# Kernel tuning notes

Hardware: AMD Instinct MI355X
Metric: run time of the kernel (lower is better)

## Reference

```python
import jax, jax.numpy as jnp
import numpy as np

WS = 7          # window size
NWIN = 3        # 2*neig_win_num+1
NH_LOC = 4      # local (POLA) heads
NH_AX = 2       # axial heads per axis
DIM = 256
LC = 128        # local channels = NH_LOC * (DIM//8)
AC = 64         # axial channels per axis
HID = 1024
B = 4
HIMG = 112
WIMG = 112
TBL = ((NWIN + 1) * WS - 1) ** 2  # 729


def _rel_pos_index():
    c = np.stack(np.meshgrid(np.arange(WS), np.arange(WS), indexing='ij')).reshape(2, -1)
    n = np.stack(np.meshgrid(np.arange(NWIN * WS), np.arange(NWIN * WS), indexing='ij')).reshape(2, -1)
    rel = (c[:, :, None] - n[:, None, :]).transpose(1, 2, 0)
    rel[..., 0] += NWIN * WS - 1
    rel[..., 1] += NWIN * WS - 1
    rel[..., 0] *= (NWIN + 1) * WS - 1
    return rel.sum(-1)  # (WS*WS, (NWIN*WS)**2)

REL_IDX = jnp.asarray(_rel_pos_index())


def _ln(x, w, b, eps=1e-5):
    mu = x.mean(-1, keepdims=True)
    var = ((x - mu) ** 2).mean(-1, keepdims=True)
    return (x - mu) * jax.lax.rsqrt(var + eps) * w + b


def _mha(q, k, v, wq, bq, wk, bk, wv, bv, wp, bp, nh, bias=None):
    Bn, Nq, C = q.shape
    d = C // nh
    qh = (q @ wq + bq).reshape(Bn, Nq, nh, d).transpose(0, 2, 1, 3) * (d ** -0.5)
    kh = (k @ wk + bk).reshape(Bn, -1, nh, d).transpose(0, 2, 1, 3)
    vh = (v @ wv + bv).reshape(Bn, -1, nh, d).transpose(0, 2, 1, 3)
    attn = jnp.einsum('bhqd,bhkd->bhqk', qh, kh)
    if bias is not None:
        attn = attn + bias[None]
    attn = jax.nn.softmax(attn, axis=-1)
    out = jnp.einsum('bhqk,bhkd->bhqd', attn, vh)
    out = out.transpose(0, 2, 1, 3).reshape(Bn, Nq, C)
    return out @ wp + bp


def _forward(x, ln1_w, ln1_b, ln2_w, ln2_b, loc_bias_table,
             loc_wq, loc_bq, loc_wk, loc_bk, loc_wv, loc_bv, loc_wp, loc_bp,
             v_wq, v_bq, v_wk, v_bk, v_wv, v_bv, v_wp, v_bp,
             h_wq, h_bq, h_wk, h_bk, h_wv, h_bv, h_wp, h_bp,
             fc1_w, fc1_b, fc2_w, fc2_b, H, W):
    Bx, L, C = x.shape
    shortcut = x
    h1 = _ln(x, ln1_w, ln1_b).reshape(Bx, H, W, C)
    xl, xv, xh = h1[..., :LC], h1[..., LC:LC + AC], h1[..., LC + AC:]
    nH, nW = H // WS, W // WS
    # --- POLA: windowed queries, 3x3-neighbor-window keys/values ---
    qw = xl.reshape(Bx, nH, WS, nW, WS, LC).transpose(0, 1, 3, 2, 4, 5).reshape(Bx * nH * nW, WS * WS, LC)
    xp = jnp.pad(xl, ((0, 0), (WS, WS), (WS, WS), (0, 0)))
    ih = (jnp.arange(nH) * WS)[:, None] + jnp.arange(NWIN * WS)[None, :]   # (nH, 3*WS)
    iw = (jnp.arange(nW) * WS)[:, None] + jnp.arange(NWIN * WS)[None, :]
    kv = xp[:, ih][:, :, :, iw]                                            # (B,nH,3ws,nW,3ws,LC)
    kv = kv.transpose(0, 1, 3, 2, 4, 5).reshape(Bx * nH * nW, (NWIN * WS) ** 2, LC)
    bias = loc_bias_table[REL_IDX].transpose(2, 0, 1)                      # (NH_LOC, 49, 441)
    ol = _mha(qw, kv, kv, loc_wq, loc_bq, loc_wk, loc_bk, loc_wv, loc_bv, loc_wp, loc_bp, NH_LOC, bias)
    ol = ol.reshape(Bx, nH, nW, WS, WS, LC).transpose(0, 1, 3, 2, 4, 5).reshape(Bx, H, W, LC)
    # --- vertical axial attention (along H, per column) ---
    xv2 = xv.transpose(0, 2, 1, 3).reshape(Bx * W, H, AC)
    ov = _mha(xv2, xv2, xv2, v_wq, v_bq, v_wk, v_bk, v_wv, v_bv, v_wp, v_bp, NH_AX)
    ov = ov.reshape(Bx, W, H, AC).transpose(0, 2, 1, 3)
    # --- horizontal axial attention (along W, per row) ---
    xh2 = xh.reshape(Bx * H, W, AC)
    oh = _mha(xh2, xh2, xh2, h_wq, h_bq, h_wk, h_bk, h_wv, h_bv, h_wp, h_bp, NH_AX)
    oh = oh.reshape(Bx, H, W, AC)
    x2 = shortcut + jnp.concatenate([ol, ov, oh], -1).reshape(Bx, L, C)
    h2 = _ln(x2, ln2_w, ln2_b)
    h2 = jax.nn.gelu(h2 @ fc1_w + fc1_b, approximate=False)
    return x2 + (h2 @ fc2_w + fc2_b)


def setup_inputs():
    key = jax.random.key(0)
    ki = iter(jax.random.split(key, 40))
    def w(shape, s=0.02):
        return jax.random.normal(next(ki), shape, jnp.float32) * s
    inp = {
        'x': jax.random.normal(next(ki), (B, HIMG * WIMG, DIM), jnp.float32),
        'H': HIMG, 'W': WIMG,
        'ln1_w': jnp.ones((DIM,), jnp.float32), 'ln1_b': jnp.zeros((DIM,), jnp.float32),
        'ln2_w': jnp.ones((DIM,), jnp.float32), 'ln2_b': jnp.zeros((DIM,), jnp.float32),
        'loc_bias_table': w((TBL, NH_LOC)),
    }
    for p, d in (('loc', LC), ('v', AC), ('h', AC)):
        for n in ('q', 'k', 'v', 'p'):
            inp[p + '_w' + n] = w((d, d))
            inp[p + '_b' + n] = w((d,))
    inp['fc1_w'] = w((DIM, HID)); inp['fc1_b'] = w((HID,))
    inp['fc2_w'] = w((HID, DIM)); inp['fc2_b'] = w((DIM,))
    return inp


def reference(x, ln1_w, ln1_b, ln2_w, ln2_b, loc_bias_table,
              loc_wq, loc_bq, loc_wk, loc_bk, loc_wv, loc_bv, loc_wp, loc_bp,
              v_wq, v_bq, v_wk, v_bk, v_wv, v_bv, v_wp, v_bp,
              h_wq, h_bq, h_wk, h_bk, h_wv, h_bv, h_wp, h_bp,
              fc1_w, fc1_b, fc2_w, fc2_b, H, W):
    return _forward(x, ln1_w, ln1_b, ln2_w, ln2_b, loc_bias_table,
                    loc_wq, loc_bq, loc_wk, loc_bk, loc_wv, loc_bv, loc_wp, loc_bp,
                    v_wq, v_bq, v_wk, v_bk, v_wv, v_bv, v_wp, v_bp,
                    h_wq, h_bq, h_wk, h_bk, h_wv, h_bv, h_wp, h_bp,
                    fc1_w, fc1_b, fc2_w, fc2_b, H, W)
```

## Files before the change

### kernel.cpp

```cpp
#include <hip/hip_runtime.h>
#include <math.h>


namespace {

constexpr int IMG  = 112;
constexpr int NTOK = 4 * IMG * IMG;
constexpr int CDIM = 256;
constexpr int LCH  = 128;
constexpr int ACH  = 64;
constexpr int HID  = 1024;
constexpr float QSC   = 0.17677669529663687f;
constexpr float LOG2E = 1.4426950408889634f;
constexpr float QSCL  = QSC * LOG2E;

typedef __attribute__((ext_vector_type(8))) short bf16x8;
typedef __attribute__((ext_vector_type(4))) float f32x4;
typedef __attribute__((ext_vector_type(2))) unsigned u32x2;

__device__ inline short f2bf(float f) {
  union { float f; unsigned u; } c; c.f = f;
  unsigned u = c.u;
  return (short)((u + 0x7fffu + ((u >> 16) & 1u)) >> 16);
}

__device__ inline bf16x8 zero8() {
  bf16x8 z;
  #pragma unroll
  for (int j = 0; j < 8; j++) z[j] = 0;
  return z;
}

__device__ inline float exp2_raw(float x) {
  float r; asm("v_exp_f32 %0, %1" : "=v"(r) : "v"(x)); return r;
}

__device__ inline float gelu_t(float x) {
  float x2 = x * x;
  float t = x * fmaf(0.0356774081f, x2, 0.7978845608f);
  t = fminf(t, 40.f);
  float u = __expf(2.f * t);
  float d = u + 1.f;
  float r;
  asm("v_rcp_f32 %0, %1" : "=v"(r) : "v"(d));
  return x * u * r;
}

__global__ __launch_bounds__(256) void conv_w_kernel(
    const float* __restrict__ src, short* __restrict__ dst, int K, int N)
{
  int idx = blockIdx.x * 256 + threadIdx.x;
  if (idx < K * N) {
    int n = idx / K, k = idx - n * K;
    dst[idx] = f2bf(src[(size_t)k * N + n]);
  }
}

__global__ __launch_bounds__(256) void conv_wp_kernel(
    const float* __restrict__ src, short* __restrict__ dst, int K, int N)
{
  int idx = blockIdx.x * 256 + threadIdx.x;
  if (idx < K * N) {
    int n = idx / K, k = idx - n * K;
    int ns = (n & ~63) | ((n & 15) << 2) | ((n >> 4) & 3);
    dst[idx] = f2bf(src[(size_t)k * N + ns]);
  }
}

__global__ __launch_bounds__(256) void loc_bias_prep(
    const float* __restrict__ btbl, float* __restrict__ biasC)
{
  int idx = blockIdx.x * 256 + threadIdx.x;
  if (idx >= 4 * 4 * 28 * 64) return;
  int lane = idx & 63;
  int t = idx >> 6;
  int n = t % 28;
  int t2 = t / 28;
  int wv = t2 & 3;
  int h = t2 >> 2;
  int l15 = lane & 15, g = lane >> 4;
  int q = wv * 16 + l15;
  if (q > 48) q = 48;
  int qy = q / 7, qx = q - qy * 7;
  #pragma unroll
  for (int r = 0; r < 4; r++) {
    int key = n * 16 + g * 4 + r;
    float val;
    if (key >= 441) {
      val = -1e30f;
    } else {
      int ky = key / 21, kx = key - ky * 21;
      val = btbl[((qy - ky + 20) * 27 + (qx - kx + 20)) * 4 + h] * LOG2E;
    }
    biasC[(size_t)idx * 4 + r] = val;
  }
}

__global__ __launch_bounds__(256) void proj_w_kernel(
    const float* __restrict__ wpl, const float* __restrict__ wpv,
    const float* __restrict__ wph,
    const float* __restrict__ bpl, const float* __restrict__ bpv,
    const float* __restrict__ bph,
    short* __restrict__ BT, float* __restrict__ pbias)
{
  int idx = blockIdx.x * 256 + threadIdx.x;
  int n = idx >> 8, k = idx & 255;
  float v = 0.f;
  if (n < 128)      { if (k < 128)             v = wpl[(size_t)k * 128 + n]; }
  else if (n < 192) { if (k >= 128 && k < 192) v = wpv[(size_t)(k - 128) * 64 + (n - 128)]; }
  else              { if (k >= 192)            v = wph[(size_t)(k - 192) * 64 + (n - 192)]; }
  BT[idx] = f2bf(v);
  if (idx < 256)
    pbias[idx] = idx < 128 ? bpl[idx] : (idx < 192 ? bpv[idx - 128] : bph[idx - 192]);
}

__global__ __launch_bounds__(256) void ln1_kernel(
    const float* __restrict__ x, const float* __restrict__ w,
    const float* __restrict__ b, short* __restrict__ out)
{
  int tok = blockIdx.x;
  int c = threadIdx.x;
  size_t idx = (size_t)tok * CDIM + c;
  float v = x[idx];
  float s = v, s2 = v * v;
  #pragma unroll
  for (int o = 32; o; o >>= 1) { s += __shfl_xor(s, o); s2 += __shfl_xor(s2, o); }
  __shared__ float red[8];
  int lane = c & 63, wv = c >> 6;
  if (lane == 0) { red[wv] = s; red[4 + wv] = s2; }
  __syncthreads();
  float a  = red[0] + red[1] + red[2] + red[3];
  float a2 = red[4] + red[5] + red[6] + red[7];
  float mu  = a * (1.f / CDIM);
  float var = a2 * (1.f / CDIM) - mu * mu;
  float rs  = rsqrtf(var + 1e-5f);
  out[idx] = f2bf((v - mu) * rs * w[c] + b[c]);
}

template<int KD, int GD>
__global__ __launch_bounds__(256) void qkv_gemm_kernel(
    const short* __restrict__ h1b, int coff, const short* __restrict__ BT,
    const float* __restrict__ bq, const float* __restrict__ bk,
    const float* __restrict__ bv,
    short* __restrict__ qo, short* __restrict__ ko, short* __restrict__ vo,
    float qscale)
{
  __shared__ short a_lds[128 * 72];
  __shared__ short b_lds[128 * 72];
  int bl = blockIdx.y * gridDim.x + blockIdx.x;
  int xcd = bl & 7, jj = bl >> 3;
  int nb = gridDim.x;
  int n0 = (jj % nb) * 128;
  int m0 = ((jj / nb) * 8 + xcd) * 128;
  int tid = threadIdx.x;
  int lane = tid & 63, wv = tid >> 6;
  int g = lane >> 4, l15 = lane & 15;
  int wm = wv >> 1, wn = wv & 1;

  f32x4 acc[4][4];
  #pragma unroll
  for (int i = 0; i < 4; i++)
    #pragma unroll
    for (int j = 0; j < 4; j++) acc[i][j] = (f32x4){0.f, 0.f, 0.f, 0.f};

  for (int kb = 0; kb < KD; kb += 64) {
    __syncthreads();
    #pragma unroll
    for (int it = 0; it < 4; it++) {
      int i = tid + it * 256;
      int row = i >> 3, c8 = i & 7;
      *(bf16x8*)&a_lds[row * 72 + c8 * 8] =
          *(const bf16x8*)&h1b[(size_t)(m0 + row) * CDIM + coff + kb + c8 * 8];
      *(bf16x8*)&b_lds[row * 72 + c8 * 8] =
          *(const bf16x8*)&BT[(size_t)(n0 + row) * KD + kb + c8 * 8];
    }
    __syncthreads();
    #pragma unroll
    for (int ks = 0; ks < 2; ks++) {
      bf16x8 af[4], bfr[4];
      #pragma unroll
      for (int i = 0; i < 4; i++)
        af[i] = *(bf16x8*)&a_lds[(wm * 64 + i * 16 + l15) * 72 + ks * 32 + g * 8];
      #pragma unroll
      for (int j = 0; j < 4; j++)
        bfr[j] = *(bf16x8*)&b_lds[(wn * 64 + j * 16 + l15) * 72 + ks * 32 + g * 8];
      #pragma unroll
      for (int i = 0; i < 4; i++)
        #pragma unroll
        for (int j = 0; j < 4; j++)
          acc[i][j] = __builtin_amdgcn_mfma_f32_16x16x32_bf16(af[i], bfr[j], acc[i][j], 0, 0, 0);
    }
  }

  int ngb = n0 + wn * 64;
  int sel = ngb / GD;
  if (sel < 3) {
    short* op = sel == 0 ? qo : (sel == 1 ? ko : vo);
    const float* bp = sel == 0 ? bq : (sel == 1 ? bk : bv);
    float sc = sel == 0 ? qscale : 1.f;
    int col = ngb - sel * GD + l15 * 4;
    f32x4 b4 = *(const f32x4*)&bp[col];
    #pragma unroll
    for (int i = 0; i < 4; i++) {
      #pragma unroll
      for (int r = 0; r < 4; r++) {
        int m = m0 + wm * 64 + i * 16 + g * 4 + r;
        float g0 = (acc[i][0][r] + b4[0]) * sc;
        float g1 = (acc[i][1][r] + b4[1]) * sc;
        float g2 = (acc[i][2][r] + b4[2]) * sc;
        float g3 = (acc[i][3][r] + b4[3]) * sc;
        unsigned p0, p1;
        asm("v_cvt_pk_bf16_f32 %0, %1, %2" : "=v"(p0) : "v"(g0), "v"(g1));
        asm("v_cvt_pk_bf16_f32 %0, %1, %2" : "=v"(p1) : "v"(g2), "v"(g3));
        u32x2 ov = {p0, p1};
        *(u32x2*)&op[(size_t)m * GD + col] = ov;
      }
    }
  }
}

__global__ __launch_bounds__(256) void loc_attn_mfma(
    const short* __restrict__ ql, const short* __restrict__ kl,
    const short* __restrict__ vl, const short* __restrict__ bkb,
    const short* __restrict__ bvb, const float* __restrict__ biasC,
    short* __restrict__ att)
{
  constexpr int KSTR = 40;
  constexpr int VSTR = 472;
  __shared__ short kv_lds[448 * KSTR];

  int head = blockIdx.x & 3;
  int wi = blockIdx.x >> 2;
  int wx = wi & 15, wy = (wi >> 4) & 15, b = wi >> 8;
  int tid = threadIdx.x;
  int lane = tid & 63, wv = tid >> 6;
  int g = lane >> 4, l15 = lane & 15;
  int hoff = head * 32;

  for (int it = tid; it < 448 * 4; it += 256) {
    int key = it >> 2, dg = it & 3;
    bf16x8 f;
    if (key < 441) {
      int ky = key / 21, kx = key - ky * 21;
      int rr = wy * 7 + ky - 7, cc = wx * 7 + kx - 7;
      if ((unsigned)rr < (unsigned)IMG && (unsigned)cc < (unsigned)IMG)
        f = *(const bf16x8*)&kl[((size_t)((b * IMG + rr) * IMG + cc)) * LCH + hoff + dg * 8];
      else
        f = *(const bf16x8*)&bkb[hoff + dg * 8];
    } else {
      f = zero8();
    }
    *(bf16x8*)(&kv_lds[key * KSTR + dg * 8]) = f;
  }

  int q0 = wv * 16 + l15;
  int qc = q0 < 49 ? q0 : 48;
  int qy0 = qc / 7, qx0 = qc - qy0 * 7;
  bf16x8 qfrag = *(const bf16x8*)&ql[((size_t)((b * IMG + wy * 7 + qy0) * IMG + wx * 7 + qx0))
                                     * LCH + hoff + g * 8];

  __syncthreads();

  const float* bptr = biasC + ((size_t)(head * 4 + wv) * 28 * 64 + lane) * 4;
  f32x4 acc[28];
  #pragma unroll
  for (int n = 0; n < 28; n++)
    acc[n] = *(const f32x4*)(bptr + n * 256);
  #pragma unroll
  for (int n = 0; n < 28; n++) {
    bf16x8 kfrag = *(bf16x8*)(&kv_lds[(n * 16 + l15) * KSTR + g * 8]);
    acc[n] = __builtin_amdgcn_mfma_f32_16x16x32_bf16(kfrag, qfrag, acc[n], 0, 0, 0);
  }

  __syncthreads();

  {
    int dgv = tid & 3;
    bool evenk = ((tid >> 2) & 1) == 0;
    #pragma unroll
    for (int k7 = 0; k7 < 7; k7++) {
      int key = (tid >> 2) + 64 * k7;
      bf16x8 v;
      if (key < 441) {
        int ky = key / 21, kx = key - ky * 21;
        int rr = wy * 7 + ky - 7, cc = wx * 7 + kx - 7;
        if ((unsigned)rr < (unsigned)IMG && (unsigned)cc < (unsigned)IMG)
          v = *(const bf16x8*)&vl[((size_t)((b * IMG + rr) * IMG + cc)) * LCH + hoff + dgv * 8];
        else
          v = *(const bf16x8*)&bvb[hoff + dgv * 8];
      } else {
        v = zero8();
      }
      union { bf16x8 v8; unsigned u[4]; } mine, other;
      mine.v8 = v;
      #pragma unroll
      for (int h = 0; h < 4; h++)
        other.u[h] = (unsigned)__shfl_xor((int)mine.u[h], 4);
      unsigned a0 = evenk ? mine.u[0] : other.u[2];
      unsigned a1 = evenk ? mine.u[1] : other.u[3];
      unsigned b0 = evenk ? other.u[0] : mine.u[2];
      unsigned b1 = evenk ? other.u[1] : mine.u[3];
      int kp0 = key & ~1;
      int kk = kp0 & 31, ch = kp0 >> 5;
      int pos = ch * 32 + ((kk & 15) >> 2) * 8 + ((kk >> 4) << 2) + (kk & 3);
      int rowbase = dgv * 8 + (evenk ? 0 : 4);
      unsigned w0 = (a0 & 0xffffu) | (b0 << 16);
      unsigned w1 = (a0 >> 16)     | (b0 & 0xffff0000u);
      unsigned w2 = (a1 & 0xffffu) | (b1 << 16);
      unsigned w3 = (a1 >> 16)     | (b1 & 0xffff0000u);
      *(unsigned*)&kv_lds[(rowbase    ) * VSTR + pos] = w0;
      *(unsigned*)&kv_lds[(rowbase + 1) * VSTR + pos] = w1;
      *(unsigned*)&kv_lds[(rowbase + 2) * VSTR + pos] = w2;
      *(unsigned*)&kv_lds[(rowbase + 3) * VSTR + pos] = w3;
    }
  }

  float m0 = -1e30f, m1 = -1e30f, m2 = -1e30f, m3 = -1e30f;
  #pragma unroll
  for (int n = 0; n < 28; n++) {
    m0 = fmaxf(m0, acc[n][0]); m1 = fmaxf(m1, acc[n][1]);
    m2 = fmaxf(m2, acc[n][2]); m3 = fmaxf(m3, acc[n][3]);
  }
  float m = fmaxf(fmaxf(m0, m1), fmaxf(m2, m3));
  m = fmaxf(m, __shfl_xor(m, 16));
  m = fmaxf(m, __shfl_xor(m, 32));
  float s0 = 0.f, s1 = 0.f, s2 = 0.f, s3 = 0.f;
  #pragma unroll
  for (int n = 0; n < 28; n++) {
    float p0 = exp2_raw(acc[n][0] - m); acc[n][0] = p0; s0 += p0;
    float p1 = exp2_raw(acc[n][1] - m); acc[n][1] = p1; s1 += p1;
    float p2 = exp2_raw(acc[n][2] - m); acc[n][2] = p2; s2 += p2;
    float p3 = exp2_raw(acc[n][3] - m); acc[n][3] = p3; s3 += p3;
  }
  float sum = (s0 + s1) + (s2 + s3);
  sum += __shfl_xor(sum, 16);
  sum += __shfl_xor(sum, 32);
  float rinv = 1.f / sum;

  __syncthreads();

  f32x4 oacc[2];
  oacc[0] = (f32x4){0.f, 0.f, 0.f, 0.f};
  oacc[1] = (f32x4){0.f, 0.f, 0.f, 0.f};
  #pragma unroll
  for (int c = 0; c < 14; c++) {
    union { unsigned u[4]; bf16x8 v8; } pk_;
    asm("v_cvt_pk_bf16_f32 %0, %1, %2" : "=v"(pk_.u[0]) : "v"(acc[2 * c][0]),     "v"(acc[2 * c][1]));
    asm("v_cvt_pk_bf16_f32 %0, %1, %2" : "=v"(pk_.u[1]) : "v"(acc[2 * c][2]),     "v"(acc[2 * c][3]));
    asm("v_cvt_pk_bf16_f32 %0, %1, %2" : "=v"(pk_.u[2]) : "v"(acc[2 * c + 1][0]), "v"(acc[2 * c + 1][1]));
    asm("v_cvt_pk_bf16_f32 %0, %1, %2" : "=v"(pk_.u[3]) : "v"(acc[2 * c + 1][2]), "v"(acc[2 * c + 1][3]));
    bf16x8 pfrag = pk_.v8;
    #pragma unroll
    for (int nt = 0; nt < 2; nt++) {
      bf16x8 vfrag = *(bf16x8*)(&kv_lds[(nt * 16 + l15) * VSTR + c * 32 + g * 8]);
      oacc[nt] = __builtin_amdgcn_mfma_f32_16x16x32_bf16(vfrag, pfrag, oacc[nt], 0, 0, 0);
    }
  }

  if (q0 < 49) {
    size_t obase = ((size_t)((b * IMG + wy * 7 + qy0) * IMG + wx * 7 + qx0)) * CDIM + hoff;
    #pragma unroll
    for (int nt = 0; nt < 2; nt++) {
      float a0 = oacc[nt][0] * rinv, a1 = oacc[nt][1] * rinv;
      float a2 = oacc[nt][2] * rinv, a3 = oacc[nt][3] * rinv;
      unsigned o0, o1;
      asm("v_cvt_pk_bf16_f32 %0, %1, %2" : "=v"(o0) : "v"(a0), "v"(a1));
      asm("v_cvt_pk_bf16_f32 %0, %1, %2" : "=v"(o1) : "v"(a2), "v"(a3));
      u32x2 ov = {o0, o1};
      *(u32x2*)&att[obase + nt * 16 + g * 4] = ov;
    }
  }
}

__global__ __launch_bounds__(256) void axial_attn_mfma(
    const short* __restrict__ q, const short* __restrict__ k,
    const short* __restrict__ v, short* __restrict__ att, int vert, int coff)
{
  constexpr int KSTR = 40;
  constexpr int VSTR = 136;
  __shared__ short k_lds[128 * KSTR];
  __shared__ short vt_lds[32 * VSTR];

  int head = blockIdx.x & 1;
  int s = blockIdx.x >> 1;
  int b = s / IMG, t = s % IMG;
  size_t base; int stride;
  if (vert) { base = ((size_t)b * IMG * IMG + t) * ACH; stride = IMG * ACH; }
  else      { base = ((size_t)(b * IMG + t)) * (size_t)IMG * ACH; stride = ACH; }
  base += head * 32;

  int tid = threadIdx.x;
  int lane = tid & 63, wv = tid >> 6;
  int g = lane >> 4, l15 = lane & 15;

  for (int it = tid; it < 448; it += 256) {
    int key = it >> 2, dg = it & 3;
    bf16x8 f = *(const bf16x8*)&k[base + (size_t)key * stride + dg * 8];
    *(bf16x8*)(&k_lds[key * KSTR + dg * 8]) = f;
  }
  {
    int dg = tid >> 6, kp = tid & 63;
    int key0 = kp * 2, key1 = key0 + 1;
    bf16x8 v0, v1;
    if (key0 < IMG) v0 = *(const bf16x8*)&v[base + (size_t)key0 * stride + dg * 8];
    else            v0 = zero8();
    if (key1 < IMG) v1 = *(const bf16x8*)&v[base + (size_t)key1 * stride + dg * 8];
    else            v1 = zero8();
    int kk = key0 & 31, ch = key0 >> 5;
    int pos = ch * 32 + ((kk & 15) >> 2) * 8 + ((kk >> 4) << 2) + (kk & 3);
    #pragma unroll
    for (int j = 0; j < 8; j++) {
      unsigned w = (unsigned short)v0[j] | ((unsigned)(unsigned short)v1[j] << 16);
      *(unsigned*)&vt_lds[(dg * 8 + j) * VSTR + pos] = w;
    }
  }
  __syncthreads();

  #pragma unroll 1
  for (int mi = 0; mi < 2; mi++) {
    int mt = wv + mi * 4;
    if (mt >= 7) break;
    int qrow = mt * 16 + l15;
    bf16x8 qfrag = *(const bf16x8*)&q[base + (size_t)qrow * stride + g * 8];

    f32x4 acc[7];
    #pragma unroll
    for (int n = 0; n < 7; n++) {
      bf16x8 kfrag = *(bf16x8*)(&k_lds[(n * 16 + l15) * KSTR + g * 8]);
      f32x4 z = {0.f, 0.f, 0.f, 0.f};
      acc[n] = __builtin_amdgcn_mfma_f32_16x16x32_bf16(kfrag, qfrag, z, 0, 0, 0);
    }

    float m0 = -1e30f, m1 = -1e30f, m2 = -1e30f, m3 = -1e30f;
    #pragma unroll
    for (int n = 0; n < 7; n++) {
      m0 = fmaxf(m0, acc[n][0]); m1 = fmaxf(m1, acc[n][1]);
      m2 = fmaxf(m2, acc[n][2]); m3 = fmaxf(m3, acc[n][3]);
    }
    float m = fmaxf(fmaxf(m0, m1), fmaxf(m2, m3));
    m = fmaxf(m, __shfl_xor(m, 16));
    m = fmaxf(m, __shfl_xor(m, 32));
    float s0 = 0.f, s1 = 0.f, s2 = 0.f, s3 = 0.f;
    #pragma unroll
    for (int n = 0; n < 7; n++) {
      float p0 = exp2_raw(acc[n][0] - m); acc[n][0] = p0; s0 += p0;
      float p1 = exp2_raw(acc[n][1] - m); acc[n][1] = p1; s1 += p1;
      float p2 = exp2_raw(acc[n][2] - m); acc[n][2] = p2; s2 += p2;
      float p3 = exp2_raw(acc[n][3] - m); acc[n][3] = p3; s3 += p3;
    }
    float sum = (s0 + s1) + (s2 + s3);
    sum += __shfl_xor(sum, 16);
    sum += __shfl_xor(sum, 32);
    float rinv = 1.f / sum;

    f32x4 oacc[2];
    oacc[0] = (f32x4){0.f, 0.f, 0.f, 0.f};
    oacc[1] = (f32x4){0.f, 0.f, 0.f, 0.f};
    #pragma unroll
    for (int c = 0; c < 4; c++) {
      union { unsigned u[4]; bf16x8 v8; } pk_;
      asm("v_cvt_pk_bf16_f32 %0, %1, %2" : "=v"(pk_.u[0]) : "v"(acc[2 * c][0]), "v"(acc[2 * c][1]));
      asm("v_cvt_pk_bf16_f32 %0, %1, %2" : "=v"(pk_.u[1]) : "v"(acc[2 * c][2]), "v"(acc[2 * c][3]));
      if (2 * c + 1 < 7) {
        asm("v_cvt_pk_bf16_f32 %0, %1, %2" : "=v"(pk_.u[2]) : "v"(acc[2 * c + 1][0]), "v"(acc[2 * c + 1][1]));
        asm("v_cvt_pk_bf16_f32 %0, %1, %2" : "=v"(pk_.u[3]) : "v"(acc[2 * c + 1][2]), "v"(acc[2 * c + 1][3]));
      } else {
        pk_.u[2] = 0; pk_.u[3] = 0;
      }
      bf16x8 pfrag = pk_.v8;
      #pragma unroll
      for (int nt = 0; nt < 2; nt++) {
        bf16x8 vfrag = *(bf16x8*)(&vt_lds[(nt * 16 + l15) * VSTR + c * 32 + g * 8]);
        oacc[nt] = __builtin_amdgcn_mfma_f32_16x16x32_bf16(vfrag, pfrag, oacc[nt], 0, 0, 0);
      }
    }

    int qq = mt * 16 + l15;
    int token = vert ? (b * IMG + qq) * IMG + t : (b * IMG + t) * IMG + qq;
    short* op = att + (size_t)token * CDIM + coff + head * 32;
    #pragma unroll
    for (int nt = 0; nt < 2; nt++) {
      float a0 = oacc[nt][0] * rinv, a1 = oacc[nt][1] * rinv;
      float a2 = oacc[nt][2] * rinv, a3 = oacc[nt][3] * rinv;
      unsigned o0, o1;
      asm("v_cvt_pk_bf16_f32 %0, %1, %2" : "=v"(o0) : "v"(a0), "v"(a1));
      asm("v_cvt_pk_bf16_f32 %0, %1, %2" : "=v"(o1) : "v"(a2), "v"(a3));
      u32x2 ov = {o0, o1};
      *(u32x2*)&op[nt * 16 + g * 4] = ov;
    }
  }
}

__global__ __launch_bounds__(256) void proj_gemm_ln2_kernel(
    const short* __restrict__ att, const short* __restrict__ BT,
    const float* __restrict__ pbias, const float* __restrict__ x,
    const float* __restrict__ lw, const float* __restrict__ lb,
    float* __restrict__ x2, short* __restrict__ n2)
{
  constexpr int TSTR = 260;
  __shared__ short smem[64 * 72 + 256 * 72];
  short* a_lds = smem;
  short* b_lds = smem + 64 * 72;
  __shared__ float lw_s[256], lb_s[256], pb_s[256];
  int m0 = blockIdx.x * 64;
  int tid = threadIdx.x;
  int lane = tid & 63, wv = tid >> 6;
  int g = lane >> 4, l15 = lane & 15;
  if (tid < 256) { lw_s[tid] = lw[tid]; lb_s[tid] = lb[tid]; pb_s[tid] = pbias[tid]; }

  f32x4 acc[16];
  #pragma unroll
  for (int n = 0; n < 16; n++) acc[n] = (f32x4){0.f, 0.f, 0.f, 0.f};

  for (int kb = 0; kb < 256; kb += 64) {
    __syncthreads();
    #pragma unroll
    for (int it = 0; it < 2; it++) {
      int i = tid + it * 256;
      int row = i >> 3, c8 = i & 7;
      *(bf16x8*)&a_lds[row * 72 + c8 * 8] =
          *(const bf16x8*)&att[(size_t)(m0 + row) * CDIM + kb + c8 * 8];
    }
    #pragma unroll
    for (int it = 0; it < 8; it++) {
      int i = tid + it * 256;
      int row = i >> 3, c8 = i & 7;
      *(bf16x8*)&b_lds[row * 72 + c8 * 8] =
          *(const bf16x8*)&BT[(size_t)row * CDIM + kb + c8 * 8];
    }
    __syncthreads();
    #pragma unroll
    for (int ks = 0; ks < 2; ks++) {
      bf16x8 af = *(bf16x8*)&a_lds[(wv * 16 + l15) * 72 + ks * 32 + g * 8];
      #pragma unroll
      for (int n = 0; n < 16; n++) {
        bf16x8 bfr = *(bf16x8*)&b_lds[(n * 16 + l15) * 72 + ks * 32 + g * 8];
        acc[n] = __builtin_amdgcn_mfma_f32_16x16x32_bf16(af, bfr, acc[n], 0, 0, 0);
      }
    }
  }

  __syncthreads();
  short* tile = smem;
  #pragma unroll
  for (int r = 0; r < 4; r++) {
    int m = m0 + wv * 16 + g * 4 + r;
    float vals[16];
    float sum = 0.f, sum2 = 0.f;
    #pragma unroll
    for (int n = 0; n < 16; n++) {
      int col = n * 16 + l15;
      float sv = acc[n][r] + pb_s[col] + x[(size_t)m * CDIM + col];
      vals[n] = sv;
      sum += sv;
      sum2 += sv * sv;
    }
    sum  += __shfl_xor(sum, 1);  sum2 += __shfl_xor(sum2, 1);
    sum  += __shfl_xor(sum, 2);  sum2 += __shfl_xor(sum2, 2);
    sum  += __shfl_xor(sum, 4);  sum2 += __shfl_xor(sum2, 4);
    sum  += __shfl_xor(sum, 8);  sum2 += __shfl_xor(sum2, 8);
    float mu  = sum * (1.f / CDIM);
    float var = sum2 * (1.f / CDIM) - mu * mu;
    float rs  = rsqrtf(var + 1e-5f);
    #pragma unroll
    for (int n = 0; n < 16; n++) {
      int col = n * 16 + l15;
      x2[(size_t)m * CDIM + col] = vals[n];
      tile[(wv * 16 + g * 4 + r) * TSTR + col] = f2bf((vals[n] - mu) * rs * lw_s[col] + lb_s[col]);
    }
  }
  __syncthreads();
  #pragma unroll
  for (int it = 0; it < 8; it++) {
    int i = it * 256 + tid;
    int row = i >> 5, c16 = i & 31;
    *(bf16x8*)&n2[(size_t)(m0 + row) * CDIM + c16 * 8] = *(bf16x8*)&tile[row * TSTR + c16 * 8];
  }
}

__global__ __launch_bounds__(256) void gemm1_gelu_kernel(
    const short* __restrict__ A, const short* __restrict__ BT,
    const float* __restrict__ b1, short* __restrict__ hid)
{
  constexpr int K = 256;
  __shared__ short a_lds[128 * 72];
  __shared__ short b_lds[128 * 72];
  int bl = blockIdx.y * gridDim.x + blockIdx.x;
  int xcd = bl & 7, jj = bl >> 3;
  int nb = gridDim.x;
  int n0 = (jj % nb) * 128;
  int m0 = ((jj / nb) * 8 + xcd) * 128;
  int tid = threadIdx.x;
  int lane = tid & 63, wv = tid >> 6;
  int g = lane >> 4, l15 = lane & 15;
  int wm = wv >> 1, wn = wv & 1;

  f32x4 acc[4][4];
  #pragma unroll
  for (int i = 0; i < 4; i++)
    #pragma unroll
    for (int j = 0; j < 4; j++) acc[i][j] = (f32x4){0.f, 0.f, 0.f, 0.f};

  for (int kb = 0; kb < K; kb += 64) {
    __syncthreads();
    #pragma unroll
    for (int it = 0; it < 4; it++) {
      int i = tid + it * 256;
      int row = i >> 3, c8 = i & 7;
      *(bf16x8*)&a_lds[row * 72 + c8 * 8] =
          *(const bf16x8*)&A[(size_t)(m0 + row) * K + kb + c8 * 8];
      *(bf16x8*)&b_lds[row * 72 + c8 * 8] =
          *(const bf16x8*)&BT[(size_t)(n0 + row) * K + kb + c8 * 8];
    }
    __syncthreads();
    #pragma unroll
    for (int ks = 0; ks < 2; ks++) {
      bf16x8 af[4], bfr[4];
      #pragma unroll
      for (int i = 0; i < 4; i++)
        af[i] = *(bf16x8*)&a_lds[(wm * 64 + i * 16 + l15) * 72 + ks * 32 + g * 8];
      #pragma unroll
      for (int j = 0; j < 4; j++)
        bfr[j] = *(bf16x8*)&b_lds[(wn * 64 + j * 16 + l15) * 72 + ks * 32 + g * 8];
      #pragma unroll
      for (int i = 0; i < 4; i++)
        #pragma unroll
        for (int j = 0; j < 4; j++)
          acc[i][j] = __builtin_amdgcn_mfma_f32_16x16x32_bf16(af[i], bfr[j], acc[i][j], 0, 0, 0);
    }
  }

  int cb = n0 + wn * 64 + l15 * 4;
  f32x4 b4 = *(const f32x4*)&b1[cb];
  #pragma unroll
  for (int i = 0; i < 4; i++) {
    #pragma unroll
    for (int r = 0; r < 4; r++) {
      int m = m0 + wm * 64 + i * 16 + g * 4 + r;
      float g0 = gelu_t(acc[i][0][r] + b4[0]);
      float g1 = gelu_t(acc[i][1][r] + b4[1]);
      float g2 = gelu_t(acc[i][2][r] + b4[2]);
      float g3 = gelu_t(acc[i][3][r] + b4[3]);
      unsigned p0, p1;
      asm("v_cvt_pk_bf16_f32 %0, %1, %2" : "=v"(p0) : "v"(g0), "v"(g1));
      asm("v_cvt_pk_bf16_f32 %0, %1, %2" : "=v"(p1) : "v"(g2), "v"(g3));
      u32x2 ov = {p0, p1};
      *(u32x2*)&hid[(size_t)m * HID + cb] = ov;
    }
  }
}

__global__ __launch_bounds__(256) void gemm2_res_kernel(
    const short* __restrict__ A, const short* __restrict__ BT,
    const float* __restrict__ b2, float* __restrict__ out)
{
  constexpr int K = 1024;
  __shared__ short a_lds[128 * 72];
  __shared__ short b_lds[128 * 72];
  int bl = blockIdx.y * gridDim.x + blockIdx.x;
  int xcd = bl & 7, jj = bl >> 3;
  int nb = gridDim.x;
  int n0 = (jj % nb) * 128;
  int m0 = ((jj / nb) * 8 + xcd) * 128;
  int tid = threadIdx.x;
  int lane = tid & 63, wv = tid >> 6;
  int g = lane >> 4, l15 = lane & 15;
  int wm = wv >> 1, wn = wv & 1;

  f32x4 acc[4][4];
  #pragma unroll
  for (int i = 0; i < 4; i++)
    #pragma unroll
    for (int j = 0; j < 4; j++) acc[i][j] = (f32x4){0.f, 0.f, 0.f, 0.f};

  for (int kb = 0; kb < K; kb += 64) {
    __syncthreads();
    #pragma unroll
    for (int it = 0; it < 4; it++) {
      int i = tid + it * 256;
      int row = i >> 3, c8 = i & 7;
      *(bf16x8*)&a_lds[row * 72 + c8 * 8] =
          *(const bf16x8*)&A[(size_t)(m0 + row) * K + kb + c8 * 8];
      *(bf16x8*)&b_lds[row * 72 + c8 * 8] =
          *(const bf16x8*)&BT[(size_t)(n0 + row) * K + kb + c8 * 8];
    }
    __syncthreads();
    #pragma unroll
    for (int ks = 0; ks < 2; ks++) {
      bf16x8 af[4], bfr[4];
      #pragma unroll
      for (int i = 0; i < 4; i++)
        af[i] = *(bf16x8*)&a_lds[(wm * 64 + i * 16 + l15) * 72 + ks * 32 + g * 8];
      #pragma unroll
      for (int j = 0; j < 4; j++)
        bfr[j] = *(bf16x8*)&b_lds[(wn * 64 + j * 16 + l15) * 72 + ks * 32 + g * 8];
      #pragma unroll
      for (int i = 0; i < 4; i++)
        #pragma unroll
        for (int j = 0; j < 4; j++)
          acc[i][j] = __builtin_amdgcn_mfma_f32_16x16x32_bf16(af[i], bfr[j], acc[i][j], 0, 0, 0);
    }
  }

  int cb = n0 + wn * 64 + l15 * 4;
  f32x4 b4 = *(const f32x4*)&b2[cb];
  #pragma unroll
  for (int i = 0; i < 4; i++) {
    #pragma unroll
    for (int r = 0; r < 4; r++) {
      int m = m0 + wm * 64 + i * 16 + g * 4 + r;
      size_t idx = (size_t)m * CDIM + cb;
      f32x4 o = *(f32x4*)&out[idx];
      o[0] += acc[i][0][r] + b4[0];
      o[1] += acc[i][1][r] + b4[1];
      o[2] += acc[i][2][r] + b4[2];
      o[3] += acc[i][3][r] + b4[3];
      *(f32x4*)&out[idx] = o;
    }
  }
}

}

extern "C" void kernel_launch(void* const* d_in, const int* in_sizes, int n_in,
                              void* d_out, int out_size, void* d_ws, size_t ws_size,
                              hipStream_t stream)
{
  const float* x    = (const float*)d_in[0];
  const float* ln1w = (const float*)d_in[3];
  const float* ln1b = (const float*)d_in[4];
  const float* ln2w = (const float*)d_in[5];
  const float* ln2b = (const float*)d_in[6];
  const float* btbl = (const float*)d_in[7];
  const float* lwq  = (const float*)d_in[8];
  const float* lbq  = (const float*)d_in[9];
  const float* lwk  = (const float*)d_in[10];
  const float* lbk  = (const float*)d_in[11];
  const float* lwv  = (const float*)d_in[12];
  const float* lbv  = (const float*)d_in[13];
  const float* lwp  = (const float*)d_in[14];
  const float* lbp  = (const float*)d_in[15];
  const float* vwq  = (const float*)d_in[16];
  const float* vbq  = (const float*)d_in[17];
  const float* vwk  = (const float*)d_in[18];
  const float* vbk  = (const float*)d_in[19];
  const float* vwv  = (const float*)d_in[20];
  const float* vbv  = (const float*)d_in[21];
  const float* vwp  = (const float*)d_in[22];
  const float* vbp  = (const float*)d_in[23];
  const float* hwq  = (const float*)d_in[24];
  const float* hbq  = (const float*)d_in[25];
  const float* hwk  = (const float*)d_in[26];
  const float* hbk  = (const float*)d_in[27];
  const float* hwv  = (const float*)d_in[28];
  const float* hbv  = (const float*)d_in[29];
  const float* hwp  = (const float*)d_in[30];
  const float* hbp  = (const float*)d_in[31];
  const float* fc1w = (const float*)d_in[32];
  const float* fc1b = (const float*)d_in[33];
  const float* fc2w = (const float*)d_in[34];
  const float* fc2b = (const float*)d_in[35];

  float* ws = (float*)d_ws;
  size_t off = 0;
  auto alloc = [&](size_t n) { float* p = ws + off; off += n; return p; };
  float* h1f = alloc((size_t)NTOK * CDIM);
  float* qls = alloc((size_t)NTOK * LCH);
  float* kls = alloc((size_t)NTOK * LCH);
  float* vls = alloc((size_t)NTOK * LCH);
  float* spare = alloc((size_t)NTOK * LCH);
  float* qvs = alloc((size_t)NTOK * ACH);
  float* kvs = alloc((size_t)NTOK * ACH);
  float* vvs = alloc((size_t)NTOK * ACH);
  float* qhs = alloc((size_t)NTOK * ACH);
  float* khs = alloc((size_t)NTOK * ACH);
  float* vhs = alloc((size_t)NTOK * ACH);
  (void)spare;
  short* w1t     = (short*)(ws + off);
  short* w2t     = w1t + (size_t)CDIM * HID;
  short* loc_bt  = w2t + (size_t)CDIM * HID;
  short* axv_bt  = loc_bt + 384 * 128;
  short* axh_bt  = axv_bt + 192 * 64;
  short* bt_proj = axh_bt + 192 * 64;
  short* bkb     = bt_proj + 256 * 256;
  short* bvb     = bkb + 128;
  float* pbias   = (float*)(bvb + 128);
  float* biasC   = pbias + 256;
  short* h1b = (short*)h1f;
  short* att = (short*)h1f;
  short* n2  = att + (size_t)NTOK * CDIM;
  short* qlb = (short*)qls; short* klb = (short*)kls; short* vlb = (short*)vls;
  short* qvb = (short*)qvs; short* kvb = (short*)kvs; short* vvb = (short*)vvs;
  short* qhb = (short*)qhs; short* khb = (short*)khs; short* vhb = (short*)vhs;
  short* hid = (short*)qls;
  float* x2  = (float*)d_out;

  conv_wp_kernel<<<(CDIM * HID + 255) / 256, 256, 0, stream>>>(fc1w, w1t, CDIM, HID);
  conv_wp_kernel<<<(CDIM * HID + 255) / 256, 256, 0, stream>>>(fc2w, w2t, HID, CDIM);
  conv_wp_kernel<<<64, 256, 0, stream>>>(lwq, loc_bt,             128, 128);
  conv_wp_kernel<<<64, 256, 0, stream>>>(lwk, loc_bt + 128*128,   128, 128);
  conv_wp_kernel<<<64, 256, 0, stream>>>(lwv, loc_bt + 2*128*128, 128, 128);
  conv_wp_kernel<<<16, 256, 0, stream>>>(vwq, axv_bt,             64, 64);
  conv_wp_kernel<<<16, 256, 0, stream>>>(vwk, axv_bt + 64*64,     64, 64);
  conv_wp_kernel<<<16, 256, 0, stream>>>(vwv, axv_bt + 2*64*64,   64, 64);
  conv_wp_kernel<<<16, 256, 0, stream>>>(hwq, axh_bt,             64, 64);
  conv_wp_kernel<<<16, 256, 0, stream>>>(hwk, axh_bt + 64*64,     64, 64);
  conv_wp_kernel<<<16, 256, 0, stream>>>(hwv, axh_bt + 2*64*64,   64, 64);
  conv_w_kernel<<<1, 256, 0, stream>>>(lbk, bkb, 1, 128);
  conv_w_kernel<<<1, 256, 0, stream>>>(lbv, bvb, 1, 128);
  proj_w_kernel<<<256, 256, 0, stream>>>(lwp, vwp, hwp, lbp, vbp, hbp, bt_proj, pbias);
  loc_bias_prep<<<112, 256, 0, stream>>>(btbl, biasC);

  ln1_kernel<<<NTOK, 256, 0, stream>>>(x, ln1w, ln1b, h1b);
  qkv_gemm_kernel<128,128><<<dim3(3, NTOK/128), 256, 0, stream>>>(
      h1b, 0, loc_bt, lbq, lbk, lbv, qlb, klb, vlb, QSCL);
  qkv_gemm_kernel<64,64><<<dim3(2, NTOK/128), 256, 0, stream>>>(
      h1b, 128, axv_bt, vbq, vbk, vbv, qvb, kvb, vvb, QSCL);
  qkv_gemm_kernel<64,64><<<dim3(2, NTOK/128), 256, 0, stream>>>(
      h1b, 192, axh_bt, hbq, hbk, hbv, qhb, khb, vhb, QSCL);
  loc_attn_mfma<<<4096, 256, 0, stream>>>(qlb, klb, vlb, bkb, bvb, biasC, att);
  axial_attn_mfma<<<896, 256, 0, stream>>>(qvb, kvb, vvb, att, 1, 128);
  axial_attn_mfma<<<896, 256, 0, stream>>>(qhb, khb, vhb, att, 0, 192);
  proj_gemm_ln2_kernel<<<NTOK / 64, 256, 0, stream>>>(att, bt_proj, pbias, x,
                                                      ln2w, ln2b, x2, n2);
  gemm1_gelu_kernel<<<dim3(HID / 128, NTOK / 128), 256, 0, stream>>>(n2, w1t, fc1b, hid);
  gemm2_res_kernel<<<dim3(CDIM / 128, NTOK / 128), 256, 0, stream>>>(hid, w2t, fc2b, x2);
}
```

Before: 535.0 us.

## Give K and transposed V separate LDS buffers and load both before the barrier

Splits the shared K/V buffer in the local-window attention kernel into separate K and transposed-V arrays, so V is loaded and transposed up front alongside K. This removes two block barriers and the mid-kernel global V gather that had to wait for the QK^T MFMAs to finish. The V transpose now writes eight scalar 32-bit words per pair of keys directly instead of using cross-lane shuffles. LDS use grows from about 36 KB to about 65 KB per block, which may reduce occupancy, and the scalar transposed stores may cause bank conflicts.

```diff
diff --git a/kernel.cpp b/kernel.cpp
--- a/kernel.cpp
+++ b/kernel.cpp
@@ -226,8 +226,9 @@
     short* __restrict__ att)
 {
   constexpr int KSTR = 40;
-  constexpr int VSTR = 472;
-  __shared__ short kv_lds[448 * KSTR];
+  constexpr int VSTR = 456;
+  __shared__ short k_lds[448 * KSTR];
+  __shared__ short vt_lds[32 * VSTR];
 
   int head = blockIdx.x & 3;
   int wi = blockIdx.x >> 2;
@@ -237,7 +238,9 @@
   int g = lane >> 4, l15 = lane & 15;
   int hoff = head * 32;
 
-  for (int it = tid; it < 448 * 4; it += 256) {
+  #pragma unroll
+  for (int ii = 0; ii < 7; ii++) {
+    int it = tid + ii * 256;
     int key = it >> 2, dg = it & 3;
     bf16x8 f;
     if (key < 441) {
@@ -250,7 +253,43 @@
     } else {
       f = zero8();
     }
-    *(bf16x8*)(&kv_lds[key * KSTR + dg * 8]) = f;
+    *(bf16x8*)(&k_lds[key * KSTR + dg * 8]) = f;
+  }
+
+  #pragma unroll
+  for (int ii = 0; ii < 4; ii++) {
+    int it = tid + ii * 256;
+    if (it < 896) {
+      int dg = it / 224;
+      int kp = it - dg * 224;
+      int key0 = kp * 2, key1 = key0 + 1;
+      bf16x8 v0, v1;
+      {
+        int ky = key0 / 21, kx = key0 - ky * 21;
+        int rr = wy * 7 + ky - 7, cc = wx * 7 + kx - 7;
+        if ((unsigned)rr < (unsigned)IMG && (unsigned)cc < (unsigned)IMG)
+          v0 = *(const bf16x8*)&vl[((size_t)((b * IMG + rr) * IMG + cc)) * LCH + hoff + dg * 8];
+        else
+          v0 = *(const bf16x8*)&bvb[hoff + dg * 8];
+      }
+      if (key1 < 441) {
+        int ky = key1 / 21, kx = key1 - ky * 21;
+        int rr = wy * 7 + ky - 7, cc = wx * 7 + kx - 7;
+        if ((unsigned)rr < (unsigned)IMG && (unsigned)cc < (unsigned)IMG)
+          v1 = *(const bf16x8*)&vl[((size_t)((b * IMG + rr) * IMG + cc)) * LCH + hoff + dg * 8];
+        else
+          v1 = *(const bf16x8*)&bvb[hoff + dg * 8];
+      } else {
+        v1 = zero8();
+      }
+      int kk = key0 & 31, ch = key0 >> 5;
+      int pos = ch * 32 + ((kk & 15) >> 2) * 8 + ((kk >> 4) << 2) + (kk & 3);
+      #pragma unroll
+      for (int j = 0; j < 8; j++) {
+        unsigned w = (unsigned short)v0[j] | ((unsigned)(unsigned short)v1[j] << 16);
+        *(unsigned*)&vt_lds[(dg * 8 + j) * VSTR + pos] = w;
+      }
+    }
   }
 
   int q0 = wv * 16 + l15;
@@ -268,51 +307,8 @@
     acc[n] = *(const f32x4*)(bptr + n * 256);
   #pragma unroll
   for (int n = 0; n < 28; n++) {
-    bf16x8 kfrag = *(bf16x8*)(&kv_lds[(n * 16 + l15) * KSTR + g * 8]);
+    bf16x8 kfrag = *(bf16x8*)(&k_lds[(n * 16 + l15) * KSTR + g * 8]);
     acc[n] = __builtin_amdgcn_mfma_f32_16x16x32_bf16(kfrag, qfrag, acc[n], 0, 0, 0);
-  }
-
-  __syncthreads();
-
-  {
-    int dgv = tid & 3;
-    bool evenk = ((tid >> 2) & 1) == 0;
-    #pragma unroll
-    for (int k7 = 0; k7 < 7; k7++) {
-      int key = (tid >> 2) + 64 * k7;
-      bf16x8 v;
-      if (key < 441) {
-        int ky = key / 21, kx = key - ky * 21;
-        int rr = wy * 7 + ky - 7, cc = wx * 7 + kx - 7;
-        if ((unsigned)rr < (unsigned)IMG && (unsigned)cc < (unsigned)IMG)
-          v = *(const bf16x8*)&vl[((size_t)((b * IMG + rr) * IMG + cc)) * LCH + hoff + dgv * 8];
-        else
-          v = *(const bf16x8*)&bvb[hoff + dgv * 8];
-      } else {
-        v = zero8();
-      }
-      union { bf16x8 v8; unsigned u[4]; } mine, other;
-      mine.v8 = v;
-      #pragma unroll
-      for (int h = 0; h < 4; h++)
-        other.u[h] = (unsigned)__shfl_xor((int)mine.u[h], 4);
-      unsigned a0 = evenk ? mine.u[0] : other.u[2];
-      unsigned a1 = evenk ? mine.u[1] : other.u[3];
-      unsigned b0 = evenk ? other.u[0] : mine.u[2];
-      unsigned b1 = evenk ? other.u[1] : mine.u[3];
-      int kp0 = key & ~1;
-      int kk = kp0 & 31, ch = kp0 >> 5;
-      int pos = ch * 32 + ((kk & 15) >> 2) * 8 + ((kk >> 4) << 2) + (kk & 3);
-      int rowbase = dgv * 8 + (evenk ? 0 : 4);
-      unsigned w0 = (a0 & 0xffffu) | (b0 << 16);
-      unsigned w1 = (a0 >> 16)     | (b0 & 0xffff0000u);
-      unsigned w2 = (a1 & 0xffffu) | (b1 << 16);
-      unsigned w3 = (a1 >> 16)     | (b1 & 0xffff0000u);
-      *(unsigned*)&kv_lds[(rowbase    ) * VSTR + pos] = w0;
-      *(unsigned*)&kv_lds[(rowbase + 1) * VSTR + pos] = w1;
-      *(unsigned*)&kv_lds[(rowbase + 2) * VSTR + pos] = w2;
-      *(unsigned*)&kv_lds[(rowbase + 3) * VSTR + pos] = w3;
-    }
   }
 
   float m0 = -1e30f, m1 = -1e30f, m2 = -1e30f, m3 = -1e30f;
@@ -336,8 +332,6 @@
   sum += __shfl_xor(sum, 16);
   sum += __shfl_xor(sum, 32);
   float rinv = 1.f / sum;
-
-  __syncthreads();
 
   f32x4 oacc[2];
   oacc[0] = (f32x4){0.f, 0.f, 0.f, 0.f};
@@ -352,7 +346,7 @@
     bf16x8 pfrag = pk_.v8;
     #pragma unroll
     for (int nt = 0; nt < 2; nt++) {
-      bf16x8 vfrag = *(bf16x8*)(&kv_lds[(nt * 16 + l15) * VSTR + c * 32 + g * 8]);
+      bf16x8 vfrag = *(bf16x8*)(&vt_lds[(nt * 16 + l15) * VSTR + c * 32 + g * 8]);
       oacc[nt] = __builtin_amdgcn_mfma_f32_16x16x32_bf16(vfrag, pfrag, oacc[nt], 0, 0, 0);
     }
   }
```

Result: no change. 528.4 us (-1.2%).
